# Kernel tuning notes

Hardware: AMD Instinct MI355X
Metric: run time of the kernel (lower is better)

Reference implementation:

```python
import jax, jax.numpy as jnp
import numpy as np

N = 50000          # nodes (multiple of p+e=8)
E = 400000         # edges (avg degree 8)
H, C = 4, 128      # heads, per-head channels
IN = 5             # input node feature dim
HID = 512          # mlp hidden dim
P, EV = 4, 4       # pursuers / evaders per graph
NEG_SLOPE = 0.2    # GATConv leaky_relu slope

# static team index: nodes with idx % (P+EV) < P  (team='pursuer')
_idx = np.arange(N)
TEAM_IDX = jnp.asarray(_idx[_idx % (P + EV) < P])  # [N/2]


def setup_inputs() -> dict:
    key = jax.random.key(0)
    ks = jax.random.split(key, 16)
    s = 0.1
    return {
        "x": jax.random.normal(ks[0], (N, IN), jnp.float32),
        "edge_index": jax.random.randint(ks[1], (2, E), 0, N, jnp.int64),
        "edge_attr": jax.random.normal(ks[2], (E, 2), jnp.float32),
        # GATConv params
        "W": jax.random.normal(ks[3], (H * C, IN), jnp.float32) * s,
        "att_src": jax.random.normal(ks[4], (H, C), jnp.float32) * s,
        "att_dst": jax.random.normal(ks[5], (H, C), jnp.float32) * s,
        "bias": jnp.zeros((H * C,), jnp.float32),
        # MLP head params
        "W1": jax.random.normal(ks[6], (HID, H * C), jnp.float32) * s,
        "b1": jnp.zeros((HID,), jnp.float32),
        "W2": jax.random.normal(ks[7], (HID, HID), jnp.float32) * s,
        "b2": jnp.zeros((HID,), jnp.float32),
        "W3": jax.random.normal(ks[8], (2, HID), jnp.float32) * s,
        "b3": jnp.zeros((2,), jnp.float32),
    }


def _gat_max(x, src, dst, W, att_src, att_dst, bias):
    # linear transform: [N, H, C]
    h = (x @ W.T).reshape(N, H, C)
    a_src = jnp.einsum("nhc,hc->nh", h, att_src)  # [N, H]
    a_dst = jnp.einsum("nhc,hc->nh", h, att_dst)  # [N, H]
    # per-edge attention logits, leaky relu
    alpha = jax.nn.leaky_relu(a_src[src] + a_dst[dst], NEG_SLOPE)  # [Et, H]
    # segment softmax over incoming edges of each dst node
    amax = jax.ops.segment_max(alpha, dst, num_segments=N)  # [N, H]
    ex = jnp.exp(alpha - amax[dst])
    den = jax.ops.segment_sum(ex, dst, num_segments=N)      # [N, H]
    attn = ex / den[dst]                                     # [Et, H]
    # alpha-weighted messages, scatter-MAX aggregation (aggr='max')
    msg = h[src] * attn[:, :, None]                          # [Et, H, C]
    out = jax.ops.segment_max(msg, dst, num_segments=N)     # [N, H, C]
    return out.reshape(N, H * C) + bias


def reference(x, edge_index, edge_attr, W, att_src, att_dst, bias,
              W1, b1, W2, b2, W3, b3):
    # PyG GATConv default add_self_loops=True; edge_attr ignored (edge_dim=None)
    loops = jnp.arange(N, dtype=edge_index.dtype)
    src = jnp.concatenate([edge_index[0], loops])
    dst = jnp.concatenate([edge_index[1], loops])
    emb = _gat_max(x, src, dst, W, att_src, att_dst, bias)  # [N, 512]
    h = emb[TEAM_IDX]                                        # [N/2, 512]
    h = jax.nn.relu(h @ W1.T + b1)
    h = jax.nn.relu(h @ W2.T + b2)
    return jnp.tanh(h @ W3.T + b3)                           # [N/2, 2]
```

## Files before the change

kernel.cpp:

```cpp
#include <hip/hip_runtime.h>
#include <hip/hip_bf16.h>
#include <math.h>

#define N_NODES 50000
#define N_EDGES 400000
#define HEADS   4
#define HC      512
#define IN_DIM  5
#define M_SEL   25000
#define NEG_SLOPE 0.2f

typedef __attribute__((ext_vector_type(8))) short bf16x8;
typedef __attribute__((ext_vector_type(4))) float f32x4;

__device__ inline unsigned short f2bf(float f) {
    union { float f; unsigned u; } v; v.f = f;
    unsigned r = v.u + 0x7FFF + ((v.u >> 16) & 1);
    return (unsigned short)(r >> 16);
}
__device__ inline float bf2f(unsigned short b) {
    union { unsigned u; float f; } v; v.u = ((unsigned)b) << 16;
    return v.f;
}

#define TR_NPW 8

__global__ __launch_bounds__(256) void k_transform(
        const float* __restrict__ x, const float* __restrict__ W,
        const float* __restrict__ att_src, const float* __restrict__ att_dst,
        unsigned short* __restrict__ h, float* __restrict__ a_src,
        float* __restrict__ a_dst, int* __restrict__ deg) {
    int wave = threadIdx.x >> 6, lane = threadIdx.x & 63;
    int c0 = lane * 8;

    float wreg[40];
    const float4* wp = (const float4*)(W + c0 * IN_DIM);
#pragma unroll
    for (int i = 0; i < 10; i++) ((float4*)wreg)[i] = wp[i];
    float sas[8], sad[8];
    *(float4*)&sas[0] = *(const float4*)(att_src + c0);
    *(float4*)&sas[4] = *(const float4*)(att_src + c0 + 4);
    *(float4*)&sad[0] = *(const float4*)(att_dst + c0);
    *(float4*)&sad[4] = *(const float4*)(att_dst + c0 + 4);

    int n0 = (blockIdx.x * 4 + wave) * TR_NPW;
#pragma unroll
    for (int t = 0; t < TR_NPW; t++) {
        int n = n0 + t;
        if (n >= N_NODES) return;
        float xv[IN_DIM];
#pragma unroll
        for (int i = 0; i < IN_DIM; i++) xv[i] = x[n * IN_DIM + i];

        float ps = 0.f, pd = 0.f;
        bf16x8 hv8;
#pragma unroll
        for (int j = 0; j < 8; j++) {
            float acc = 0.f;
#pragma unroll
            for (int i = 0; i < IN_DIM; i++) acc += xv[i] * wreg[j * IN_DIM + i];
            hv8[j] = (short)f2bf(acc);
            ps += acc * sas[j];
            pd += acc * sad[j];
        }
        *(bf16x8*)(h + (size_t)n * HC + c0) = hv8;

#pragma unroll
        for (int off = 8; off >= 1; off >>= 1) {
            ps += __shfl_xor(ps, off);
            pd += __shfl_xor(pd, off);
        }
        if ((lane & 15) == 0) {
            int head = lane >> 4;
            a_src[n * HEADS + head] = ps;
            a_dst[n * HEADS + head] = pd;
        }
        if (lane == 0) deg[n] = 1;
    }
}

__global__ void k_hist(const int* __restrict__ ei, int* __restrict__ deg) {
    int e = blockIdx.x * 256 + threadIdx.x;
    if (e < N_EDGES) atomicAdd(&deg[ei[N_EDGES + e]], 1);
}

#define NSCAN_BLK 196

__global__ void k_scan1(const int* __restrict__ deg, int* __restrict__ excl,
                        int* __restrict__ bsum) {
    __shared__ int s[256];
    int i = blockIdx.x * 256 + threadIdx.x;
    int v = (i < N_NODES) ? deg[i] : 0;
    s[threadIdx.x] = v;
    __syncthreads();
    for (int off = 1; off < 256; off <<= 1) {
        int t = (threadIdx.x >= off) ? s[threadIdx.x - off] : 0;
        __syncthreads();
        s[threadIdx.x] += t;
        __syncthreads();
    }
    if (i < N_NODES) excl[i] = s[threadIdx.x] - v;
    if (threadIdx.x == 255) bsum[blockIdx.x] = s[255];
}

__global__ void k_scan3fill(const int* __restrict__ excl, const int* __restrict__ bsum,
                            int* __restrict__ offs, int* __restrict__ curs,
                            int* __restrict__ csr) {
    __shared__ int part[256];
    int tid = threadIdx.x;
    part[tid] = (tid < NSCAN_BLK) ? bsum[tid] : 0;
    __syncthreads();
    for (int off = 1; off < 256; off <<= 1) {
        int t = (tid >= off) ? part[tid - off] : 0;
        __syncthreads();
        part[tid] += t;
        __syncthreads();
    }
    int blockoff = (blockIdx.x == 0) ? 0 : part[blockIdx.x - 1];
    int i = blockIdx.x * 256 + tid;
    if (i < N_NODES) {
        int o = excl[i] + blockoff;
        offs[i] = o;
        csr[o] = i;
        curs[i] = o + 1;
    }
}

__global__ void k_fill_edges(const int* __restrict__ ei, int* __restrict__ cursor,
                             int* __restrict__ csr) {
    int e = blockIdx.x * 256 + threadIdx.x;
    if (e < N_EDGES) {
        int d = ei[N_EDGES + e];
        int pos = atomicAdd(&cursor[d], 1);
        csr[pos] = ei[e];
    }
}

__global__ __launch_bounds__(256, 4) void k_aggregate(
        const unsigned short* __restrict__ h, const float* __restrict__ a_src,
        const float* __restrict__ a_dst, const int* __restrict__ csr,
        const int* __restrict__ offs, const int* __restrict__ deg,
        const float* __restrict__ bias, unsigned short* __restrict__ emb_sel) {
    int wave = threadIdx.x >> 6, lane = threadIdx.x & 63;
    int w = blockIdx.x * 4 + wave;
    if (w >= M_SEL) return;
    int n = ((w >> 2) << 3) + (w & 3);

    int base = offs[n];
    int dn = deg[n];
    int head = lane >> 4, egrp = lane & 15;
    int c0 = lane * 8;

    float acc[8];
#pragma unroll
    for (int j = 0; j < 8; j++) acc[j] = -INFINITY;

    if (dn <= 16) {
        int slot = (egrp < dn) ? egrp : (dn - 1);
        int s_e = csr[base + slot];
        float adn = a_dst[n * HEADS + head];
        float araw = a_src[s_e * HEADS + head];

        bf16x8 v[16];
#pragma unroll
        for (int e = 0; e < 16; e++) {
            int s = __shfl(s_e, e);
            v[e] = *(const bf16x8*)(h + (size_t)s * HC + c0);
        }
        __builtin_amdgcn_sched_barrier(0);

        float t = araw + adn;
        t = (t > 0.f) ? t : NEG_SLOPE * t;
        if (egrp >= dn) t = -INFINITY;
        float m = t;
#pragma unroll
        for (int off = 8; off >= 1; off >>= 1) m = fmaxf(m, __shfl_xor(m, off));
        float ex = (egrp < dn) ? __expf(t - m) : 0.f;
        float den = ex;
#pragma unroll
        for (int off = 8; off >= 1; off >>= 1) den += __shfl_xor(den, off);
        float attn = ex / den;

#pragma unroll
        for (int e = 0; e < 16; e++) {
            if (e < dn) {
                float a = __shfl(attn, (head << 4) | e);
#pragma unroll
                for (int j = 0; j < 8; j++)
                    acc[j] = fmaxf(acc[j], bf2f((unsigned short)v[e][j]) * a);
            }
        }
    } else {
        float adn = a_dst[n * HEADS + head];
        float m = -INFINITY;
        for (int e0 = 0; e0 < dn; e0 += 16) {
            int e = e0 + egrp;
            if (e < dn) {
                int s = csr[base + e];
                float t = a_src[s * HEADS + head] + adn;
                t = (t > 0.f) ? t : NEG_SLOPE * t;
                m = fmaxf(m, t);
            }
        }
#pragma unroll
        for (int off = 8; off >= 1; off >>= 1) m = fmaxf(m, __shfl_xor(m, off));
        float den = 0.f;
        for (int e0 = 0; e0 < dn; e0 += 16) {
            int e = e0 + egrp;
            if (e < dn) {
                int s = csr[base + e];
                float t = a_src[s * HEADS + head] + adn;
                t = (t > 0.f) ? t : NEG_SLOPE * t;
                den += __expf(t - m);
            }
        }
#pragma unroll
        for (int off = 8; off >= 1; off >>= 1) den += __shfl_xor(den, off);
        float invden = 1.0f / den;
        for (int e = 0; e < dn; e++) {
            int s = csr[base + e];
            float t = a_src[s * HEADS + head] + adn;
            t = (t > 0.f) ? t : NEG_SLOPE * t;
            float attn = __expf(t - m) * invden;
            bf16x8 hv = *(const bf16x8*)(h + (size_t)s * HC + c0);
#pragma unroll
            for (int j = 0; j < 8; j++)
                acc[j] = fmaxf(acc[j], bf2f((unsigned short)hv[j]) * attn);
        }
    }

    bf16x8 ov;
#pragma unroll
    for (int j = 0; j < 8; j++) ov[j] = (short)f2bf(acc[j] + bias[c0 + j]);
    *(bf16x8*)(emb_sel + (size_t)w * HC + c0) = ov;
}

#define BK  64
#define LDK 72

__device__ inline bf16x8 cvt8(float4 a, float4 b) {
    bf16x8 r;
    r[0] = (short)f2bf(a.x); r[1] = (short)f2bf(a.y);
    r[2] = (short)f2bf(a.z); r[3] = (short)f2bf(a.w);
    r[4] = (short)f2bf(b.x); r[5] = (short)f2bf(b.y);
    r[6] = (short)f2bf(b.z); r[7] = (short)f2bf(b.w);
    return r;
}

template <int MODE>
__global__ __launch_bounds__(512, 2) void k_gemm(const unsigned short* __restrict__ A, int M,
                                                 const float* __restrict__ Wt,
                                                 const float* __restrict__ bias,
                                                 unsigned short* __restrict__ C,
                                                 const float* __restrict__ W3,
                                                 float* __restrict__ part) {
    __shared__ unsigned short As[256 * LDK];
    __shared__ unsigned short Bs[256 * LDK];
    int tid = threadIdx.x;
    int m0 = blockIdx.y * 256;
    int o0 = blockIdx.x * 256;
    int wv = tid >> 6, lane = tid & 63;
    int wm = wv >> 1, wn = wv & 1;

    f32x4 acc[4][8];
#pragma unroll
    for (int i = 0; i < 4; i++)
#pragma unroll
        for (int j = 0; j < 8; j++) acc[i][j] = (f32x4){0.f, 0.f, 0.f, 0.f};

    bf16x8 ra[4], rb[4];
#pragma unroll
    for (int s = 0; s < 4; s++) {
        int c = s * 512 + tid;
        int row = c >> 3, col = (c & 7) * 8;
        int m = m0 + row;
        bf16x8 av = {0, 0, 0, 0, 0, 0, 0, 0};
        if (m < M) av = *(const bf16x8*)(A + (size_t)m * HC + col);
        ra[s] = av;
        const float4* wp = (const float4*)(Wt + (size_t)(o0 + row) * HC + col);
        rb[s] = cvt8(wp[0], wp[1]);
    }

    for (int k0 = 0; k0 < HC; k0 += BK) {
        __syncthreads();
#pragma unroll
        for (int s = 0; s < 4; s++) {
            int c = s * 512 + tid;
            int row = c >> 3, col = (c & 7) * 8;
            *(bf16x8*)(&As[row * LDK + col]) = ra[s];
            *(bf16x8*)(&Bs[row * LDK + col]) = rb[s];
        }
        __syncthreads();

        int kn = k0 + BK;
        if (kn < HC) {
#pragma unroll
            for (int s = 0; s < 4; s++) {
                int c = s * 512 + tid;
                int row = c >> 3, col = (c & 7) * 8;
                int m = m0 + row;
                bf16x8 av = {0, 0, 0, 0, 0, 0, 0, 0};
                if (m < M) av = *(const bf16x8*)(A + (size_t)m * HC + kn + col);
                ra[s] = av;
                const float4* wp = (const float4*)(Wt + (size_t)(o0 + row) * HC + kn + col);
                rb[s] = cvt8(wp[0], wp[1]);
            }
        }

#pragma unroll
        for (int kk = 0; kk < 2; kk++) {
            int kb = kk * 32 + (lane >> 4) * 8;
            bf16x8 af[4], bfr[8];
#pragma unroll
            for (int mi = 0; mi < 4; mi++)
                af[mi] = *(const bf16x8*)(&As[(wm * 64 + mi * 16 + (lane & 15)) * LDK + kb]);
#pragma unroll
            for (int ni = 0; ni < 8; ni++)
                bfr[ni] = *(const bf16x8*)(&Bs[(wn * 128 + ni * 16 + (lane & 15)) * LDK + kb]);
#pragma unroll
            for (int mi = 0; mi < 4; mi++)
#pragma unroll
                for (int ni = 0; ni < 8; ni++)
                    acc[mi][ni] = __builtin_amdgcn_mfma_f32_16x16x32_bf16(
                        af[mi], bfr[ni], acc[mi][ni], 0, 0, 0);
        }
    }

    if (MODE == 0) {
#pragma unroll
        for (int ni = 0; ni < 8; ni++) {
            int ncol = o0 + wn * 128 + ni * 16 + (lane & 15);
            float bv = bias[ncol];
#pragma unroll
            for (int mi = 0; mi < 4; mi++) {
                int mbase = m0 + wm * 64 + mi * 16 + (lane >> 4) * 4;
#pragma unroll
                for (int r = 0; r < 4; r++) {
                    int m = mbase + r;
                    if (m < M) {
                        float v = fmaxf(acc[mi][ni][r] + bv, 0.f);
                        C[(size_t)m * HC + ncol] = f2bf(v);
                    }
                }
            }
        }
    } else {
        float p0[4][4], p1[4][4];
#pragma unroll
        for (int mi = 0; mi < 4; mi++)
#pragma unroll
            for (int r = 0; r < 4; r++) { p0[mi][r] = 0.f; p1[mi][r] = 0.f; }
#pragma unroll
        for (int ni = 0; ni < 8; ni++) {
            int ncol = o0 + wn * 128 + ni * 16 + (lane & 15);
            float bv = bias[ncol];
            float w0 = W3[ncol], w1 = W3[HC + ncol];
#pragma unroll
            for (int mi = 0; mi < 4; mi++)
#pragma unroll
                for (int r = 0; r < 4; r++) {
                    float v = fmaxf(acc[mi][ni][r] + bv, 0.f);
                    p0[mi][r] += v * w0;
                    p1[mi][r] += v * w1;
                }
        }
#pragma unroll
        for (int mi = 0; mi < 4; mi++)
#pragma unroll
            for (int r = 0; r < 4; r++) {
                float a0 = p0[mi][r], a1 = p1[mi][r];
#pragma unroll
                for (int off = 8; off >= 1; off >>= 1) {
                    a0 += __shfl_xor(a0, off);
                    a1 += __shfl_xor(a1, off);
                }
                int m = m0 + wm * 64 + mi * 16 + (lane >> 4) * 4 + r;
                if ((lane & 15) == 0 && m < M) {
                    atomicAdd(&part[m * 2 + 0], a0);
                    atomicAdd(&part[m * 2 + 1], a1);
                }
            }
    }
}

__global__ void k_tanh(const float* __restrict__ part, const float* __restrict__ b3,
                       float* __restrict__ out) {
    int i = blockIdx.x * 256 + threadIdx.x;
    if (i < 2 * M_SEL) out[i] = tanhf(part[i] + b3[i & 1]);
}

extern "C" void kernel_launch(void* const* d_in, const int* in_sizes, int n_in,
                              void* d_out, int out_size, void* d_ws, size_t ws_size,
                              hipStream_t stream) {
    const float* x       = (const float*)d_in[0];
    const int*   ei      = (const int*)d_in[1];
    const float* W       = (const float*)d_in[3];
    const float* att_src = (const float*)d_in[4];
    const float* att_dst = (const float*)d_in[5];
    const float* bias    = (const float*)d_in[6];
    const float* W1      = (const float*)d_in[7];
    const float* b1      = (const float*)d_in[8];
    const float* W2      = (const float*)d_in[9];
    const float* b2      = (const float*)d_in[10];
    const float* W3      = (const float*)d_in[11];
    const float* b3      = (const float*)d_in[12];
    float* out = (float*)d_out;

    char* ws = (char*)d_ws;
    unsigned short* h       = (unsigned short*)(ws);
    unsigned short* emb_sel = (unsigned short*)(ws + 51200000);
    unsigned short* h1      = (unsigned short*)(ws + 76800000);
    float* part  = (float*)(ws + 102400000);
    float* a_src = (float*)(ws + 129048576);
    float* a_dst = (float*)(ws + 129848576);
    int*   deg   = (int*)  (ws + 130648576);
    int*   offs  = (int*)  (ws + 130848576);
    int*   curs  = (int*)  (ws + 131048576);
    int*   excl  = (int*)  (ws + 131248576);
    int*   bsum  = (int*)  (ws + 131448576);
    int*   csr   = (int*)  (ws + 131449600);

    hipMemsetAsync(part, 0, 2 * M_SEL * sizeof(float), stream);
    k_transform<<<(N_NODES + 31) / 32, 256, 0, stream>>>(x, W, att_src, att_dst, h,
                                                         a_src, a_dst, deg);
    k_hist<<<(N_EDGES + 255) / 256, 256, 0, stream>>>(ei, deg);
    k_scan1<<<NSCAN_BLK, 256, 0, stream>>>(deg, excl, bsum);
    k_scan3fill<<<NSCAN_BLK, 256, 0, stream>>>(excl, bsum, offs, curs, csr);
    k_fill_edges<<<(N_EDGES + 255) / 256, 256, 0, stream>>>(ei, curs, csr);
    k_aggregate<<<6250, 256, 0, stream>>>(h, a_src, a_dst, csr, offs, deg, bias, emb_sel);

    dim3 g(2, 98);
    k_gemm<0><<<g, 512, 0, stream>>>(emb_sel, M_SEL, W1, b1, h1, nullptr, nullptr);
    k_gemm<1><<<g, 512, 0, stream>>>(h1, M_SEL, W2, b2, nullptr, W3, part);
    k_tanh<<<196, 256, 0, stream>>>(part, b3, out);
}
```

Baseline: 191.1 us.

## Recompute node features from x in aggregation instead of storing h

Stops writing the 50000x512 bf16 projected feature matrix h in the transform kernel. The aggregate kernel now keeps W in registers and recomputes each neighbor's 8 channels from its 5 input features on the fly. This removes roughly 51 MB of writes plus the gathered reads of h, at the cost of extra FMAs per edge and small uncoalesced reads of x. Aggregation now uses full fp32 values rather than bf16-rounded h, and the workspace layout is compacted.

Measured after the change: 198.5 us. 3.9% more time.

```diff
diff --git a/kernel.cpp b/kernel.cpp
--- a/kernel.cpp
+++ b/kernel.cpp
@@ -28,8 +28,7 @@
 __global__ __launch_bounds__(256) void k_transform(
         const float* __restrict__ x, const float* __restrict__ W,
         const float* __restrict__ att_src, const float* __restrict__ att_dst,
-        unsigned short* __restrict__ h, float* __restrict__ a_src,
-        float* __restrict__ a_dst, int* __restrict__ deg) {
+        float* __restrict__ a_src, float* __restrict__ a_dst, int* __restrict__ deg) {
     int wave = threadIdx.x >> 6, lane = threadIdx.x & 63;
     int c0 = lane * 8;
 
@@ -53,18 +52,14 @@
         for (int i = 0; i < IN_DIM; i++) xv[i] = x[n * IN_DIM + i];
 
         float ps = 0.f, pd = 0.f;
-        bf16x8 hv8;
 #pragma unroll
         for (int j = 0; j < 8; j++) {
             float acc = 0.f;
 #pragma unroll
             for (int i = 0; i < IN_DIM; i++) acc += xv[i] * wreg[j * IN_DIM + i];
-            hv8[j] = (short)f2bf(acc);
             ps += acc * sas[j];
             pd += acc * sad[j];
         }
-        *(bf16x8*)(h + (size_t)n * HC + c0) = hv8;
-
 #pragma unroll
         for (int off = 8; off >= 1; off >>= 1) {
             ps += __shfl_xor(ps, off);
@@ -137,13 +132,13 @@
 }
 
 __global__ __launch_bounds__(256, 4) void k_aggregate(
-        const unsigned short* __restrict__ h, const float* __restrict__ a_src,
-        const float* __restrict__ a_dst, const int* __restrict__ csr,
-        const int* __restrict__ offs, const int* __restrict__ deg,
-        const float* __restrict__ bias, unsigned short* __restrict__ emb_sel) {
+        const float* __restrict__ x, const float* __restrict__ W,
+        const float* __restrict__ a_src, const float* __restrict__ a_dst,
+        const int* __restrict__ csr, const int* __restrict__ offs,
+        const int* __restrict__ deg, const float* __restrict__ bias,
+        unsigned short* __restrict__ emb_sel) {
     int wave = threadIdx.x >> 6, lane = threadIdx.x & 63;
     int w = blockIdx.x * 4 + wave;
-    if (w >= M_SEL) return;
     int n = ((w >> 2) << 3) + (w & 3);
 
     int base = offs[n];
@@ -151,6 +146,11 @@
     int head = lane >> 4, egrp = lane & 15;
     int c0 = lane * 8;
 
+    float wreg[40];
+    const float4* wp = (const float4*)(W + c0 * IN_DIM);
+#pragma unroll
+    for (int i = 0; i < 10; i++) ((float4*)wreg)[i] = wp[i];
+
     float acc[8];
 #pragma unroll
     for (int j = 0; j < 8; j++) acc[j] = -INFINITY;
@@ -159,35 +159,29 @@
         int slot = (egrp < dn) ? egrp : (dn - 1);
         int s_e = csr[base + slot];
         float adn = a_dst[n * HEADS + head];
-        float araw = a_src[s_e * HEADS + head];
-
-        bf16x8 v[16];
-#pragma unroll
-        for (int e = 0; e < 16; e++) {
-            int s = __shfl(s_e, e);
-            v[e] = *(const bf16x8*)(h + (size_t)s * HC + c0);
-        }
-        __builtin_amdgcn_sched_barrier(0);
-
-        float t = araw + adn;
-        t = (t > 0.f) ? t : NEG_SLOPE * t;
-        if (egrp >= dn) t = -INFINITY;
-        float m = t;
+        float tl = a_src[s_e * HEADS + head] + adn;
+        tl = (tl > 0.f) ? tl : NEG_SLOPE * tl;
+        if (egrp >= dn) tl = -INFINITY;
+        float m = tl;
 #pragma unroll
         for (int off = 8; off >= 1; off >>= 1) m = fmaxf(m, __shfl_xor(m, off));
-        float ex = (egrp < dn) ? __expf(t - m) : 0.f;
+        float ex = (egrp < dn) ? __expf(tl - m) : 0.f;
         float den = ex;
 #pragma unroll
         for (int off = 8; off >= 1; off >>= 1) den += __shfl_xor(den, off);
         float attn = ex / den;
 
-#pragma unroll
-        for (int e = 0; e < 16; e++) {
-            if (e < dn) {
-                float a = __shfl(attn, (head << 4) | e);
-#pragma unroll
-                for (int j = 0; j < 8; j++)
-                    acc[j] = fmaxf(acc[j], bf2f((unsigned short)v[e][j]) * a);
+        for (int e = 0; e < dn; e++) {
+            int s = __shfl(s_e, e);
+            float a = __shfl(attn, (head << 4) | e);
+            const float* xp = x + s * IN_DIM;
+            float x0 = xp[0], x1 = xp[1], x2 = xp[2], x3 = xp[3], x4 = xp[4];
+#pragma unroll
+            for (int j = 0; j < 8; j++) {
+                float hv = x0 * wreg[j * 5 + 0] + x1 * wreg[j * 5 + 1]
+                         + x2 * wreg[j * 5 + 2] + x3 * wreg[j * 5 + 3]
+                         + x4 * wreg[j * 5 + 4];
+                acc[j] = fmaxf(acc[j], hv * a);
             }
         }
     } else {
@@ -222,10 +216,15 @@
             float t = a_src[s * HEADS + head] + adn;
             t = (t > 0.f) ? t : NEG_SLOPE * t;
             float attn = __expf(t - m) * invden;
-            bf16x8 hv = *(const bf16x8*)(h + (size_t)s * HC + c0);
-#pragma unroll
-            for (int j = 0; j < 8; j++)
-                acc[j] = fmaxf(acc[j], bf2f((unsigned short)hv[j]) * attn);
+            const float* xp = x + s * IN_DIM;
+            float x0 = xp[0], x1 = xp[1], x2 = xp[2], x3 = xp[3], x4 = xp[4];
+#pragma unroll
+            for (int j = 0; j < 8; j++) {
+                float hv = x0 * wreg[j * 5 + 0] + x1 * wreg[j * 5 + 1]
+                         + x2 * wreg[j * 5 + 2] + x3 * wreg[j * 5 + 3]
+                         + x4 * wreg[j * 5 + 4];
+                acc[j] = fmaxf(acc[j], hv * attn);
+            }
         }
     }
 
@@ -407,27 +406,26 @@
     float* out = (float*)d_out;
 
     char* ws = (char*)d_ws;
-    unsigned short* h       = (unsigned short*)(ws);
-    unsigned short* emb_sel = (unsigned short*)(ws + 51200000);
-    unsigned short* h1      = (unsigned short*)(ws + 76800000);
-    float* part  = (float*)(ws + 102400000);
-    float* a_src = (float*)(ws + 129048576);
-    float* a_dst = (float*)(ws + 129848576);
-    int*   deg   = (int*)  (ws + 130648576);
-    int*   offs  = (int*)  (ws + 130848576);
-    int*   curs  = (int*)  (ws + 131048576);
-    int*   excl  = (int*)  (ws + 131248576);
-    int*   bsum  = (int*)  (ws + 131448576);
-    int*   csr   = (int*)  (ws + 131449600);
+    unsigned short* emb_sel = (unsigned short*)(ws);
+    unsigned short* h1      = (unsigned short*)(ws + 25600000);
+    float* part  = (float*)(ws + 51400000);
+    float* a_src = (float*)(ws + 51600000);
+    float* a_dst = (float*)(ws + 52400000);
+    int*   deg   = (int*)  (ws + 53200000);
+    int*   offs  = (int*)  (ws + 53400000);
+    int*   curs  = (int*)  (ws + 53600000);
+    int*   excl  = (int*)  (ws + 53800000);
+    int*   bsum  = (int*)  (ws + 54000000);
+    int*   csr   = (int*)  (ws + 54001024);
 
     hipMemsetAsync(part, 0, 2 * M_SEL * sizeof(float), stream);
-    k_transform<<<(N_NODES + 31) / 32, 256, 0, stream>>>(x, W, att_src, att_dst, h,
+    k_transform<<<(N_NODES + 31) / 32, 256, 0, stream>>>(x, W, att_src, att_dst,
                                                          a_src, a_dst, deg);
     k_hist<<<(N_EDGES + 255) / 256, 256, 0, stream>>>(ei, deg);
     k_scan1<<<NSCAN_BLK, 256, 0, stream>>>(deg, excl, bsum);
     k_scan3fill<<<NSCAN_BLK, 256, 0, stream>>>(excl, bsum, offs, curs, csr);
     k_fill_edges<<<(N_EDGES + 255) / 256, 256, 0, stream>>>(ei, curs, csr);
-    k_aggregate<<<6250, 256, 0, stream>>>(h, a_src, a_dst, csr, offs, deg, bias, emb_sel);
+    k_aggregate<<<6250, 256, 0, stream>>>(x, W, a_src, a_dst, csr, offs, deg, bias, emb_sel);
 
     dim3 g(2, 98);
     k_gemm<0><<<g, 512, 0, stream>>>(emb_sel, M_SEL, W1, b1, h1, nullptr, nullptr);
```
